# Kernel optimization log

Hardware: AMD Instinct MI355X
Metric: run time of the kernel (lower is better)

## Reference

```python
import jax, jax.numpy as jnp
import numpy as np

N, E = 50000, 800000
IN_CH, H, OUT_CH, ED, L = 64, 128, 128, 1, 4


def setup_inputs() -> dict:
    key = jax.random.key(0)
    ks = jax.random.split(key, 24)
    s = 0.02
    inp = {
        'h': jax.random.normal(ks[0], (N, IN_CH), jnp.float32),
        'coords': jax.random.normal(ks[1], (N, 3), jnp.float32),
        'edge_attr': jax.random.normal(ks[2], (E, ED), jnp.float32),
        'emb_in_W': jax.random.normal(ks[3], (IN_CH, H), jnp.float32) * s,
        'emb_in_b': jnp.zeros((H,), jnp.float32),
        'emb_out_W': jax.random.normal(ks[4], (H, OUT_CH), jnp.float32) * s,
        'emb_out_b': jnp.zeros((OUT_CH,), jnp.float32),
        # per-layer stacked params
        'eW1': jax.random.normal(ks[5], (L, 2 * H + 1 + ED, H), jnp.float32) * s,
        'eb1': jnp.zeros((L, H), jnp.float32),
        'eW2': jax.random.normal(ks[6], (L, H, H), jnp.float32) * s,
        'eb2': jnp.zeros((L, H), jnp.float32),
        'cW1': jax.random.normal(ks[7], (L, H, H), jnp.float32) * s,
        'cb1': jnp.zeros((L, H), jnp.float32),
        'cWc': jax.random.normal(ks[8], (L, H, 1), jnp.float32) * 0.001,  # xavier gain=0.001, no bias
        'nW1': jax.random.normal(ks[9], (L, 2 * H, H), jnp.float32) * s,
        'nb1': jnp.zeros((L, H), jnp.float32),
        'nW2': jax.random.normal(ks[10], (L, H, H), jnp.float32) * s,
        'nb2': jnp.zeros((L, H), jnp.float32),
        'edge_index': jax.random.randint(ks[11], (2, E), 0, N, jnp.int32),
    }
    return inp


def _egnn_forward(h, coords, edge_attr, emb_in_W, emb_in_b, emb_out_W, emb_out_b,
                  eW1, eb1, eW2, eb2, cW1, cb1, cWc, nW1, nb1, nW2, nb2, edge_index):
    silu = jax.nn.silu
    row, col = edge_index[0], edge_index[1]  # PyG: j=source=row, i=target=col
    # count of incoming edges per target node, for coords_agg='mean'
    counts = jax.ops.segment_sum(jnp.ones((E,), jnp.float32), col, num_segments=N)
    counts = jnp.maximum(counts, 1.0)[:, None]
    h = h @ emb_in_W + emb_in_b
    for l in range(L):
        coord_diff = coords[row] - coords[col]                       # [E,3]
        dist = jnp.sum(coord_diff * coord_diff, axis=-1, keepdims=True)  # [E,1]
        # message: edge MLP on cat(x_i, x_j, dist, edge_attr)
        edge_in = jnp.concatenate([h[col], h[row], dist, edge_attr], axis=-1)
        ef = silu(edge_in @ eW1[l] + eb1[l])
        ef = silu(ef @ eW2[l] + eb2[l])                               # [E,H]
        cw = silu(ef @ cW1[l] + cb1[l]) @ cWc[l]                      # [E,1]
        coord_upd = coord_diff * cw                                   # [E,3]
        # aggregate to target nodes
        agg_feat = jax.ops.segment_sum(ef, col, num_segments=N)       # [N,H]
        agg_coord = jax.ops.segment_sum(coord_upd, col, num_segments=N) / counts
        # node update (residual)
        node_in = jnp.concatenate([h, agg_feat], axis=-1)
        upd = silu(node_in @ nW1[l] + nb1[l]) @ nW2[l] + nb2[l]
        h = h + upd
        coords = coords + agg_coord
    h = h @ emb_out_W + emb_out_b
    return h, coords


def reference(h, coords, edge_attr, emb_in_W, emb_in_b, emb_out_W, emb_out_b,
              eW1, eb1, eW2, eb2, cW1, cb1, cWc, nW1, nb1, nW2, nb2, edge_index):
    return _egnn_forward(h, coords, edge_attr, emb_in_W, emb_in_b, emb_out_W, emb_out_b,
                         eW1, eb1, eW2, eb2, cW1, cb1, cWc, nW1, nb1, nW2, nb2, edge_index)
```

## Files before the change

kernel.cpp:

```cpp
#include <hip/hip_runtime.h>

constexpr int Nn = 50000;
constexpr int Ee = 800000;
constexpr int EF_STR  = 136;
constexpr int NIN_STR = 264;
constexpr int HIN_STR = 72;
constexpr int NB_SCAN = (Nn + 255) / 256;

typedef short s8v __attribute__((ext_vector_type(8)));
typedef float f4v __attribute__((ext_vector_type(4)));

__device__ __forceinline__ ushort f2bf(float f) {
    uint u = __float_as_uint(f);
    uint r = (u + 0x7FFFu + ((u >> 16) & 1u)) >> 16;
    return (ushort)r;
}
__device__ __forceinline__ ushort f2bf_t(float f) {
    return (ushort)(__float_as_uint(f) >> 16);
}
__device__ __forceinline__ float bf2f(ushort s) {
    return __uint_as_float(((uint)s) << 16);
}
__device__ __forceinline__ float silu_f(float x) {
    return x * __fdividef(1.0f, 1.0f + __expf(-x));
}
__device__ __forceinline__ uint pack2bf_t(float lo, float hi) {
    return __builtin_amdgcn_perm(__float_as_uint(hi), __float_as_uint(lo), 0x07060302u);
}
__device__ __forceinline__ uint pack2bf_r(float lo, float hi) {
    uint a = __float_as_uint(lo) + 0x8000u;
    uint b = __float_as_uint(hi) + 0x8000u;
    return __builtin_amdgcn_perm(b, a, 0x07060302u);
}

__device__ __forceinline__ void swz_one(const float* src, ushort* dst, int K, int lstride, int KC, int idx)
{
    int per = KC * 4096;
    int l = idx / per, r = idx % per;
    int fb = r >> 9, rem = r & 511;
    int lane = rem >> 3, jj = rem & 7;
    int kc = fb >> 3, t = fb & 7;
    int k = kc * 32 + ((lane >> 4) << 3) + jj;
    int n = t * 16 + (lane & 15);
    float v = (k < K) ? src[(size_t)l * lstride + (size_t)k * 128 + n] : 0.0f;
    dst[idx] = f2bf(v);
}
__global__ void __launch_bounds__(256) k_swz_all(
    const float* __restrict__ eW1, const float* __restrict__ eW2, const float* __restrict__ cW1,
    const float* __restrict__ nW1, const float* __restrict__ nW2,
    const float* __restrict__ inW, const float* __restrict__ outW,
    ushort* __restrict__ oT, ushort* __restrict__ oM,
    ushort* __restrict__ o2, ushort* __restrict__ o3,
    ushort* __restrict__ o4, ushort* __restrict__ o5,
    ushort* __restrict__ o6, ushort* __restrict__ o7)
{
    int gid = blockIdx.x * 256 + threadIdx.x;
    if (gid < 65536)       swz_one(eW1,         oT, 128, 33024, 4, gid);
    else if (gid < 131072) swz_one(eW1 + 16384, oM, 128, 33024, 4, gid - 65536);
    else if (gid < 196608) swz_one(eW2, o2, 128, 16384, 4, gid - 131072);
    else if (gid < 262144) swz_one(cW1, o3, 128, 16384, 4, gid - 196608);
    else if (gid < 393216) swz_one(nW1, o4, 256, 32768, 8, gid - 262144);
    else if (gid < 458752) swz_one(nW2, o5, 128, 16384, 4, gid - 393216);
    else if (gid < 466944) swz_one(inW, o6, 64, 8192, 2, gid - 458752);
    else if (gid < 483328) swz_one(outW, o7, 128, 16384, 4, gid - 466944);
}

__global__ void __launch_bounds__(256) k_count(const int* __restrict__ eidx, int* __restrict__ ecnt)
{
    int e = blockIdx.x * 256 + threadIdx.x;
    atomicAdd(&ecnt[eidx[Ee + e]], 1);
}

__global__ void __launch_bounds__(256) k_bsum(const int* __restrict__ ecnt, int* __restrict__ bsum)
{
    __shared__ int ws[4];
    int tid = threadIdx.x, lane = tid & 63, w = tid >> 6;
    int i = blockIdx.x * 256 + tid;
    int x = (i < Nn) ? ecnt[i] : 0;
    #pragma unroll
    for (int off = 1; off < 64; off <<= 1) x += __shfl_xor(x, off, 64);
    if (lane == 0) ws[w] = x;
    __syncthreads();
    if (tid == 0) bsum[blockIdx.x] = ws[0] + ws[1] + ws[2] + ws[3];
}
__global__ void __launch_bounds__(256) k_bscan(int* __restrict__ bsum)
{
    __shared__ int ws[4];
    int tid = threadIdx.x, lane = tid & 63, w = tid >> 6;
    int x = (tid < NB_SCAN) ? bsum[tid] : 0;
    int s = x;
    #pragma unroll
    for (int off = 1; off < 64; off <<= 1) {
        int t = __shfl_up(s, off, 64);
        if (lane >= off) s += t;
    }
    if (lane == 63) ws[w] = s;
    __syncthreads();
    if (tid == 0) { int a = 0; for (int k = 0; k < 4; k++) { int t = ws[k]; ws[k] = a; a += t; } }
    __syncthreads();
    int excl = ws[w] + s - x;
    if (tid < NB_SCAN) bsum[tid] = excl;
}
__global__ void __launch_bounds__(256) k_cursor(const int* __restrict__ ecnt,
                                               const int* __restrict__ boff, int* __restrict__ cursor)
{
    __shared__ int ws[4];
    int tid = threadIdx.x, lane = tid & 63, w = tid >> 6;
    int i = blockIdx.x * 256 + tid;
    int x = (i < Nn) ? ecnt[i] : 0;
    int s = x;
    #pragma unroll
    for (int off = 1; off < 64; off <<= 1) {
        int t = __shfl_up(s, off, 64);
        if (lane >= off) s += t;
    }
    if (lane == 63) ws[w] = s;
// ... 75 lines not shown
            }
        }
    }
}

__global__ void __launch_bounds__(512, 2) k_uv(
    const ushort* __restrict__ hbf,
    const ushort* __restrict__ topW, const ushort* __restrict__ midW,
    const float* __restrict__ b1, ushort* __restrict__ uvb)
{
    __shared__ alignas(16) ushort s_h[64 * EF_STR];
    const int tid = threadIdx.x;
    const int nb = blockIdx.x * 64;
    #pragma unroll
    for (int i = 0; i < 2; i++) {
        int idx = i * 512 + tid;
        int e = idx >> 4, ch = idx & 15;
        int node = nb + e;
        uint4 v = make_uint4(0, 0, 0, 0);
        if (node < Nn) v = *(const uint4*)(hbf + (size_t)node * 128 + ch * 8);
        *(uint4*)(s_h + e * EF_STR + ch * 8) = v;
    }
    __syncthreads();
    const int lane = tid & 63, wave = tid >> 6;
    const int m = lane & 15, quad = lane >> 4;
    const int ws2 = wave >> 2, wt = wave & 3;
    const int rbase = ws2 * 32;
    f4v au[2][2], av[2][2];
    #pragma unroll
    for (int ct = 0; ct < 2; ct++) {
        float4 bb = *(const float4*)(b1 + (wt * 2 + ct) * 16 + quad * 4);
        au[0][ct] = (f4v){bb.x, bb.y, bb.z, bb.w};
        au[1][ct] = au[0][ct];
        av[0][ct] = (f4v){0,0,0,0};
        av[1][ct] = (f4v){0,0,0,0};
    }
    const ushort* tBase = topW + wt * 1024 + (size_t)lane * 8;
    const ushort* mBase = midW + wt * 1024 + (size_t)lane * 8;
    #pragma unroll
    for (int kc = 0; kc < 4; kc++) {
        s8v t0 = *(const s8v*)(tBase + kc * 4096);
        s8v t1 = *(const s8v*)(tBase + kc * 4096 + 512);
        s8v m0 = *(const s8v*)(mBase + kc * 4096);
        s8v m1 = *(const s8v*)(mBase + kc * 4096 + 512);
        #pragma unroll
        for (int nt = 0; nt < 2; nt++) {
            s8v bf = *(const s8v*)(s_h + (rbase + nt * 16 + m) * EF_STR + kc * 32 + quad * 8);
            au[nt][0] = __builtin_amdgcn_mfma_f32_16x16x32_bf16(t0, bf, au[nt][0], 0, 0, 0);
            au[nt][1] = __builtin_amdgcn_mfma_f32_16x16x32_bf16(t1, bf, au[nt][1], 0, 0, 0);
            av[nt][0] = __builtin_amdgcn_mfma_f32_16x16x32_bf16(m0, bf, av[nt][0], 0, 0, 0);
            av[nt][1] = __builtin_amdgcn_mfma_f32_16x16x32_bf16(m1, bf, av[nt][1], 0, 0, 0);
        }
    }
    #pragma unroll
    for (int nt = 0; nt < 2; nt++) {
        int node = nb + rbase + nt * 16 + m;
        if (node < Nn) {
            #pragma unroll
            for (int ct = 0; ct < 2; ct++) {
                int colb = (wt * 2 + ct) * 16 + quad * 4;
                uint2 pu; pu.x = pack2bf_r(au[nt][ct][0], au[nt][ct][1]);
                          pu.y = pack2bf_r(au[nt][ct][2], au[nt][ct][3]);
                *(uint2*)(uvb + (size_t)node * 256 + colb) = pu;
                uint2 pv; pv.x = pack2bf_r(av[nt][ct][0], av[nt][ct][1]);
                          pv.y = pack2bf_r(av[nt][ct][2], av[nt][ct][3]);
                *(uint2*)(uvb + (size_t)node * 256 + 128 + colb) = pv;
            }
        }
    }
}

__device__ __forceinline__ uint uv_term(uint uw, uint vw, float dist, float attr,
                                        const float* wdp, const float* wap, int j)
{
    float2 w2d = *(const float2*)(wdp + 2 * j);
    float2 w2a = *(const float2*)(wap + 2 * j);
    float lo = __uint_as_float(uw << 16) + __uint_as_float(vw << 16)
             + dist * w2d.x + attr * w2a.x;
    float hi = __uint_as_float(uw & 0xFFFF0000u) + __uint_as_float(vw & 0xFFFF0000u)
             + dist * w2d.y + attr * w2a.y;
    return pack2bf_t(silu_f(lo), silu_f(hi));
}

__global__ void __launch_bounds__(512, 8) k_edge(
    const float* __restrict__ cbuf,
    const int* __restrict__ srow, const int* __restrict__ scol, const float* __restrict__ sattr,
    const ushort* __restrict__ uvb,
    const float* __restrict__ wd, const float* __restrict__ wa,
    const ushort* __restrict__ w2s, const float* __restrict__ b2,
    const ushort* __restrict__ cw1s, const float* __restrict__ cb1,
    const float* __restrict__ cwc,
    float* __restrict__ agg_feat, float* __restrict__ agg_coord)
{
    __shared__ alignas(16) ushort s_a[64 * EF_STR];
    __shared__ alignas(16) ushort s_b[64 * EF_STR];
    __shared__ alignas(16) float  s_t[64 * 20];
    __shared__ int   s_col[64];
    __shared__ float s_cd[64 * 3];

    const int tid = threadIdx.x;
    const int eb = blockIdx.x * 64;

    const int e = tid >> 3, ch = tid & 7;
    const int myrow = srow[eb + e];
    const int mycol = scol[eb + e];
    const float attr = sattr[eb + e];
    const ushort* up = uvb + (size_t)mycol * 256 + ch * 16;
    const ushort* vp = uvb + (size_t)myrow * 256 + 128 + ch * 16;
    uint4 ua = *(const uint4*)up;
    uint4 ub = *(const uint4*)(up + 8);
    uint4 va = *(const uint4*)vp;
    uint4 vb = *(const uint4*)(vp + 8);

    if (tid < 64) {
        int rw = srow[eb + tid], cl = scol[eb + tid];
        s_col[tid] = cl;
        float d0 = cbuf[rw * 3 + 0] - cbuf[cl * 3 + 0];
        float d1 = cbuf[rw * 3 + 1] - cbuf[cl * 3 + 1];
        float d2 = cbuf[rw * 3 + 2] - cbuf[cl * 3 + 2];
        s_cd[tid * 3 + 0] = d0; s_cd[tid * 3 + 1] = d1; s_cd[tid * 3 + 2] = d2;
        s_t[tid * 20 + 16] = d0 * d0 + d1 * d1 + d2 * d2;
    }
    __syncthreads();

    {
        const float dist = s_t[e * 20 + 16];
        const float* wdp = wd + ch * 16;
        const float* wap = wa + ch * 16;
        uint4 q0, q1;
        q0.x = uv_term(ua.x, va.x, dist, attr, wdp, wap, 0);
        q0.y = uv_term(ua.y, va.y, dist, attr, wdp, wap, 1);
        q0.z = uv_term(ua.z, va.z, dist, attr, wdp, wap, 2);
        q0.w = uv_term(ua.w, va.w, dist, attr, wdp, wap, 3);
        *(uint4*)(s_a + e * EF_STR + ch * 16) = q0;
        q1.x = uv_term(ub.x, vb.x, dist, attr, wdp, wap, 4);
        q1.y = uv_term(ub.y, vb.y, dist, attr, wdp, wap, 5);
        q1.z = uv_term(ub.z, vb.z, dist, attr, wdp, wap, 6);
        q1.w = uv_term(ub.w, vb.w, dist, attr, wdp, wap, 7);
        *(uint4*)(s_a + e * EF_STR + ch * 16 + 8) = q1;
    }
    __syncthreads();

    const int lane = tid & 63, wave = tid >> 6;
    const int m = lane & 15, quad = lane >> 4;
    const int ws2 = wave >> 2, wt = wave & 3;
    const int rbase = ws2 * 32;

    {
        f4v acc2[2][2];
        #pragma unroll
        for (int tt = 0; tt < 2; tt++) {
            float4 bb = *(const float4*)(b2 + (wt * 2 + tt) * 16 + quad * 4);
            acc2[0][tt] = (f4v){bb.x, bb.y, bb.z, bb.w};
            acc2[1][tt] = acc2[0][tt];
        }
        const ushort* bBase = w2s + wt * 1024 + (size_t)lane * 8;
        #pragma unroll
        for (int kc = 0; kc < 4; kc++) {
            s8v b0 = *(const s8v*)(bBase + kc * 4096);
            s8v b1v = *(const s8v*)(bBase + kc * 4096 + 512);
            #pragma unroll
            for (int mt = 0; mt < 2; mt++) {
                s8v a = *(const s8v*)(s_a + (rbase + mt * 16 + m) * EF_STR + kc * 32 + quad * 8);
                acc2[mt][0] = __builtin_amdgcn_mfma_f32_16x16x32_bf16(b0, a, acc2[mt][0], 0, 0, 0);
                acc2[mt][1] = __builtin_amdgcn_mfma_f32_16x16x32_bf16(b1v, a, acc2[mt][1], 0, 0, 0);
            }
        }
        #pragma unroll
        for (int mt = 0; mt < 2; mt++)
            #pragma unroll
            for (int tt = 0; tt < 2; tt++) {
                uint2 pk;
                pk.x = pack2bf_t(silu_f(acc2[mt][tt][0]), silu_f(acc2[mt][tt][1]));
                pk.y = pack2bf_t(silu_f(acc2[mt][tt][2]), silu_f(acc2[mt][tt][3]));
                *(uint2*)(s_b + (rbase + mt * 16 + m) * EF_STR + (wt * 2 + tt) * 16 + quad * 4) = pk;
            }
    }
    __syncthreads();

    {
        f4v acc3[2][2];
        #pragma unroll
        for (int tt = 0; tt < 2; tt++) {
            float4 bb = *(const float4*)(cb1 + (wt * 2 + tt) * 16 + quad * 4);
            acc3[0][tt] = (f4v){bb.x, bb.y, bb.z, bb.w};
            acc3[1][tt] = acc3[0][tt];
        }
        const ushort* bBase = cw1s + wt * 1024 + (size_t)lane * 8;
        #pragma unroll
        for (int kc = 0; kc < 4; kc++) {
            s8v b0 = *(const s8v*)(bBase + kc * 4096);
            s8v b1v = *(const s8v*)(bBase + kc * 4096 + 512);
            #pragma unroll
            for (int mt = 0; mt < 2; mt++) {
                s8v a = *(const s8v*)(s_b + (rbase + mt * 16 + m) * EF_STR + kc * 32 + quad * 8);
                acc3[mt][0] = __builtin_amdgcn_mfma_f32_16x16x32_bf16(b0, a, acc3[mt][0], 0, 0, 0);
                acc3[mt][1] = __builtin_amdgcn_mfma_f32_16x16x32_bf16(b1v, a, acc3[mt][1], 0, 0, 0);
            }
        }
        float p0 = 0.0f, p1 = 0.0f;
        #pragma unroll
        for (int tt = 0; tt < 2; tt++) {
            float4 wc = *(const float4*)(cwc + (wt * 2 + tt) * 16 + quad * 4);
            p0 += silu_f(acc3[0][tt][0]) * wc.x + silu_f(acc3[0][tt][1]) * wc.y
                + silu_f(acc3[0][tt][2]) * wc.z + silu_f(acc3[0][tt][3]) * wc.w;
            p1 += silu_f(acc3[1][tt][0]) * wc.x + silu_f(acc3[1][tt][1]) * wc.y
                + silu_f(acc3[1][tt][2]) * wc.z + silu_f(acc3[1][tt][3]) * wc.w;
        }
        p0 += __shfl_xor(p0, 16, 64);
        p0 += __shfl_xor(p0, 32, 64);
        p1 += __shfl_xor(p1, 16, 64);
        p1 += __shfl_xor(p1, 32, 64);
        if (quad == 0) {
            s_t[(rbase + m) * 20 + wt] = p0;
            s_t[(rbase + 16 + m) * 20 + wt] = p1;
        }
    }
    __syncthreads();

    if (tid < 64) {
        float cw = s_t[tid * 20 + 0] + s_t[tid * 20 + 1] + s_t[tid * 20 + 2] + s_t[tid * 20 + 3];
        int cn = s_col[tid];
        unsafeAtomicAdd(&agg_coord[cn * 3 + 0], s_cd[tid * 3 + 0] * cw);
        unsafeAtomicAdd(&agg_coord[cn * 3 + 1], s_cd[tid * 3 + 1] * cw);
        unsafeAtomicAdd(&agg_coord[cn * 3 + 2], s_cd[tid * 3 + 2] * cw);
    }
    {
        int j = tid & 127;
        int e0 = (tid >> 7) * 16;
        float accv = 0.0f; int cur = s_col[e0];
        #pragma unroll 4
        for (int ee = e0; ee < e0 + 16; ee++) {
            int c = s_col[ee];
            if (c != cur) {
                unsafeAtomicAdd(&agg_feat[(size_t)cur * 128 + j], accv);
                accv = 0.0f; cur = c;
            }
            accv += bf2f(s_b[ee * EF_STR + j]);
        }
        unsafeAtomicAdd(&agg_feat[(size_t)cur * 128 + j], accv);
    }
}

__global__ void __launch_bounds__(512, 6) k_node(
    float* __restrict__ hbuf, ushort* __restrict__ hbf, float* __restrict__ cbuf,
    float* __restrict__ agg_feat, float* __restrict__ agg_coord,
    const int* __restrict__ ecnt,
    const ushort* __restrict__ w1s, const float* __restrict__ b1,
    const ushort* __restrict__ w2s, const float* __restrict__ b2)
{
    __shared__ alignas(16) ushort s_nin[64 * NIN_STR];
    __shared__ alignas(16) ushort s_t1[64 * EF_STR];
    const int tid = threadIdx.x;
    const int nb = blockIdx.x * 64;

    #pragma unroll
    for (int i = 0; i < 2; i++) {
        int idx = i * 512 + tid;
        int e = idx >> 4, ch = idx & 15;
        int node = nb + e;
        uint4 v = make_uint4(0, 0, 0, 0);
        if (node < Nn) v = *(const uint4*)(hbf + (size_t)node * 128 + ch * 8);
        *(uint4*)(s_nin + e * NIN_STR + ch * 8) = v;
    }
    #pragma unroll
    for (int i = 0; i < 4; i++) {
        int idx = i * 512 + tid;
        int e = idx >> 5, ch = idx & 31;
        int node = nb + e;
        float4 f = make_float4(0.f, 0.f, 0.f, 0.f);
        if (node < Nn) {
            f = *(const float4*)(agg_feat + (size_t)node * 128 + ch * 4);
            *(float4*)(agg_feat + (size_t)node * 128 + ch * 4) = make_float4(0.f, 0.f, 0.f, 0.f);
        }
        uint2 pk; pk.x = pack2bf_t(f.x, f.y); pk.y = pack2bf_t(f.z, f.w);
        *(uint2*)(s_nin + e * NIN_STR + 128 + ch * 4) = pk;
    }
    if (tid < 64) {
        int n = nb + tid;
        if (n < Nn) {
            float c = (float)ecnt[n]; c = (c < 1.0f) ? 1.0f : c;
            float inv = __fdividef(1.0f, c);
            cbuf[n * 3 + 0] += agg_coord[n * 3 + 0] * inv;
            cbuf[n * 3 + 1] += agg_coord[n * 3 + 1] * inv;
            cbuf[n * 3 + 2] += agg_coord[n * 3 + 2] * inv;
            agg_coord[n * 3 + 0] = 0.f; agg_coord[n * 3 + 1] = 0.f; agg_coord[n * 3 + 2] = 0.f;
        }
    }
    __syncthreads();

    const int lane = tid & 63, wave = tid >> 6;
    const int m = lane & 15, quad = lane >> 4;
    const int ws2 = wave >> 2, wt = wave & 3;
    const int rbase = ws2 * 32;

    {
        f4v acc[2][2];
        #pragma unroll
        for (int ct = 0; ct < 2; ct++) {
            float4 bb = *(const float4*)(b1 + (wt * 2 + ct) * 16 + quad * 4);
            acc[0][ct] = (f4v){bb.x, bb.y, bb.z, bb.w};
            acc[1][ct] = acc[0][ct];
        }
        const ushort* aBase = w1s + wt * 1024 + (size_t)lane * 8;
        #pragma unroll
        for (int kc = 0; kc < 8; kc++) {
            s8v a0 = *(const s8v*)(aBase + kc * 4096);
            s8v a1 = *(const s8v*)(aBase + kc * 4096 + 512);
            #pragma unroll
            for (int nt = 0; nt < 2; nt++) {
                s8v bf = *(const s8v*)(s_nin + (rbase + nt * 16 + m) * NIN_STR + kc * 32 + quad * 8);
                acc[nt][0] = __builtin_amdgcn_mfma_f32_16x16x32_bf16(a0, bf, acc[nt][0], 0, 0, 0);
                acc[nt][1] = __builtin_amdgcn_mfma_f32_16x16x32_bf16(a1, bf, acc[nt][1], 0, 0, 0);
            }
        }
        #pragma unroll
        for (int nt = 0; nt < 2; nt++) {
            int row = rbase + nt * 16 + m;
            #pragma unroll
            for (int ct = 0; ct < 2; ct++) {
                int colb = (wt * 2 + ct) * 16 + quad * 4;
                float v0 = silu_f(acc[nt][ct][0]);
                float v1 = silu_f(acc[nt][ct][1]);
// ... 97 lines not shown
        if (node < Nn) {
            #pragma unroll
            for (int ct = 0; ct < 2; ct++) {
                int colb = (wt * 2 + ct) * 16 + quad * 4;
                float4 o = make_float4(acc[nt][ct][0], acc[nt][ct][1],
                                       acc[nt][ct][2], acc[nt][ct][3]);
                *(float4*)(out + (size_t)node * 128 + colb) = o;
            }
        }
    }
}

extern "C" void kernel_launch(void* const* d_in, const int* in_sizes, int n_in,
                              void* d_out, int out_size, void* d_ws, size_t ws_size,
                              hipStream_t stream)
{
    const float* h_in      = (const float*)d_in[0];
    const float* coords    = (const float*)d_in[1];
    const float* edge_attr = (const float*)d_in[2];
    const float* emb_in_W  = (const float*)d_in[3];
    const float* emb_in_b  = (const float*)d_in[4];
    const float* emb_out_W = (const float*)d_in[5];
    const float* emb_out_b = (const float*)d_in[6];
    const float* eW1 = (const float*)d_in[7];
    const float* eb1 = (const float*)d_in[8];
    const float* eW2 = (const float*)d_in[9];
    const float* eb2 = (const float*)d_in[10];
    const float* cW1 = (const float*)d_in[11];
    const float* cb1 = (const float*)d_in[12];
    const float* cWc = (const float*)d_in[13];
    const float* nW1 = (const float*)d_in[14];
    const float* nb1 = (const float*)d_in[15];
    const float* nW2 = (const float*)d_in[16];
    const float* nb2 = (const float*)d_in[17];
    const int*  eidx = (const int*)d_in[18];

    size_t off = 0;
    char* base = (char*)d_ws;
    auto alloc = [&](size_t bytes) -> char* {
        char* p = base + off;
        off += (bytes + 255) & ~(size_t)255;
        return p;
    };
    float*  hbuf      = (float*)alloc((size_t)Nn * 128 * 4);
    ushort* hbf       = (ushort*)alloc((size_t)Nn * 128 * 2);
    ushort* uvb       = (ushort*)alloc((size_t)Nn * 256 * 2);
    float*  cbuf      = (float*)alloc((size_t)Nn * 3 * 4);
    int*    ecnt      = (int*)alloc((size_t)Nn * 4);
    int*    cursor    = (int*)alloc((size_t)Nn * 4);
    int*    bsum      = (int*)alloc((size_t)NB_SCAN * 4);
    int*    srow      = (int*)alloc((size_t)Ee * 4);
    int*    scol      = (int*)alloc((size_t)Ee * 4);
    float*  sattr     = (float*)alloc((size_t)Ee * 4);
    float*  agg_feat  = (float*)alloc((size_t)Nn * 128 * 4);
    float*  agg_coord = (float*)alloc((size_t)Nn * 3 * 4);
    ushort* eW1tops   = (ushort*)alloc((size_t)4 * 16384 * 2);
    ushort* eW1mids   = (ushort*)alloc((size_t)4 * 16384 * 2);
    ushort* eW2s      = (ushort*)alloc((size_t)4 * 16384 * 2);
    ushort* cW1s      = (ushort*)alloc((size_t)4 * 16384 * 2);
    ushort* nW1s      = (ushort*)alloc((size_t)4 * 32768 * 2);
    ushort* nW2s      = (ushort*)alloc((size_t)4 * 16384 * 2);
    ushort* eInWs     = (ushort*)alloc((size_t)8192 * 2);
    ushort* eOutWs    = (ushort*)alloc((size_t)16384 * 2);

    k_swz_all<<<483328 / 256, 256, 0, stream>>>(
        eW1, eW2, cW1, nW1, nW2, emb_in_W, emb_out_W,
        eW1tops, eW1mids, eW2s, cW1s, nW1s, nW2s, eInWs, eOutWs);

    hipMemsetAsync(ecnt, 0, (size_t)Nn * 4, stream);
    k_count<<<Ee / 256, 256, 0, stream>>>(eidx, ecnt);
    k_bsum<<<NB_SCAN, 256, 0, stream>>>(ecnt, bsum);
    k_bscan<<<1, 256, 0, stream>>>(bsum);
    k_cursor<<<NB_SCAN, 256, 0, stream>>>(ecnt, bsum, cursor);
    k_scatter<<<Ee / 256, 256, 0, stream>>>(eidx, edge_attr, cursor, srow, scol, sattr);
    k_emb<<<(Nn + 63) / 64, 512, 0, stream>>>(h_in, coords, eInWs, emb_in_b, hbuf, hbf, cbuf);

    hipMemsetAsync(agg_feat, 0, (size_t)Nn * 128 * 4, stream);
    hipMemsetAsync(agg_coord, 0, (size_t)Nn * 3 * 4, stream);

    for (int l = 0; l < 4; l++) {
        k_uv<<<(Nn + 63) / 64, 512, 0, stream>>>(
            hbf, eW1tops + (size_t)l * 16384, eW1mids + (size_t)l * 16384,
            eb1 + l * 128, uvb);
        k_edge<<<Ee / 64, 512, 0, stream>>>(
            cbuf, srow, scol, sattr, uvb,
            eW1 + ((size_t)l * 258 + 256) * 128,
            eW1 + ((size_t)l * 258 + 257) * 128,
            eW2s + (size_t)l * 16384, eb2 + l * 128,
            cW1s + (size_t)l * 16384, cb1 + l * 128,
            cWc + l * 128,
            agg_feat, agg_coord);
        k_node<<<(Nn + 63) / 64, 512, 0, stream>>>(
            hbuf, hbf, cbuf, agg_feat, agg_coord, ecnt,
            nW1s + (size_t)l * 32768, nb1 + l * 128,
            nW2s + (size_t)l * 16384, nb2 + l * 128);
    }
    k_emb_out<<<(Nn + 63) / 64, 512, 0, stream>>>(hbf, cbuf, eOutWs, emb_out_b, (float*)d_out);
}
```

Before: 1.642 ms.

## Make edge kernel persistent and prefetch next tile's gathers during compute

The edge kernel becomes a persistent grid-stride loop over 64-edge tiles, launched with a fixed 2048 blocks. Each iteration issues the next tile's index, coordinate and uv gathers into registers, so global latency overlaps the current tile's MFMA work. Per-tile metadata (target column, coordinate diffs) is double-buffered in shared memory, and the barriers become lighter LDS-only waits. The risks are higher register pressure (launch bounds lowered from 8 to 6), lower occupancy, and some tail imbalance, since 12500 tiles do not divide evenly over 2048 blocks.

```diff
diff --git a/kernel.cpp b/kernel.cpp
--- a/kernel.cpp
+++ b/kernel.cpp
@@ -32,6 +32,9 @@
     uint b = __float_as_uint(hi) + 0x8000u;
     return __builtin_amdgcn_perm(b, a, 0x07060302u);
 }
+
+#define LBAR() do { asm volatile("s_waitcnt lgkmcnt(0)" ::: "memory"); \
+                    __builtin_amdgcn_s_barrier(); } while (0)
 
 __device__ __forceinline__ void swz_one(const float* src, ushort* dst, int K, int lstride, int KC, int idx)
 {
@@ -273,7 +276,7 @@
     return pack2bf_t(silu_f(lo), silu_f(hi));
 }
 
-__global__ void __launch_bounds__(512, 8) k_edge(
+__global__ void __launch_bounds__(512, 6) k_edge(
     const float* __restrict__ cbuf,
     const int* __restrict__ srow, const int* __restrict__ scol, const float* __restrict__ sattr,
     const ushort* __restrict__ uvb,
@@ -285,151 +288,170 @@
 {
     __shared__ alignas(16) ushort s_a[64 * EF_STR];
     __shared__ alignas(16) ushort s_b[64 * EF_STR];
-    __shared__ alignas(16) float  s_t[64 * 20];
-    __shared__ int   s_col[64];
-    __shared__ float s_cd[64 * 3];
+    __shared__ alignas(16) float  s_t[64 * 4];
+    __shared__ int   s_col[2][64];
+    __shared__ float s_cd[2][64 * 3];
 
     const int tid = threadIdx.x;
-    const int eb = blockIdx.x * 64;
-
     const int e = tid >> 3, ch = tid & 7;
-    const int myrow = srow[eb + e];
-    const int mycol = scol[eb + e];
-    const float attr = sattr[eb + e];
-    const ushort* up = uvb + (size_t)mycol * 256 + ch * 16;
-    const ushort* vp = uvb + (size_t)myrow * 256 + 128 + ch * 16;
-    uint4 ua = *(const uint4*)up;
-    uint4 ub = *(const uint4*)(up + 8);
-    uint4 va = *(const uint4*)vp;
-    uint4 vb = *(const uint4*)(vp + 8);
-
-    if (tid < 64) {
-        int rw = srow[eb + tid], cl = scol[eb + tid];
-        s_col[tid] = cl;
-        float d0 = cbuf[rw * 3 + 0] - cbuf[cl * 3 + 0];
-        float d1 = cbuf[rw * 3 + 1] - cbuf[cl * 3 + 1];
-        float d2 = cbuf[rw * 3 + 2] - cbuf[cl * 3 + 2];
-        s_cd[tid * 3 + 0] = d0; s_cd[tid * 3 + 1] = d1; s_cd[tid * 3 + 2] = d2;
-        s_t[tid * 20 + 16] = d0 * d0 + d1 * d1 + d2 * d2;
-    }
-    __syncthreads();
-
-    {
-        const float dist = s_t[e * 20 + 16];
-        const float* wdp = wd + ch * 16;
-        const float* wap = wa + ch * 16;
-        uint4 q0, q1;
-        q0.x = uv_term(ua.x, va.x, dist, attr, wdp, wap, 0);
-        q0.y = uv_term(ua.y, va.y, dist, attr, wdp, wap, 1);
-        q0.z = uv_term(ua.z, va.z, dist, attr, wdp, wap, 2);
-        q0.w = uv_term(ua.w, va.w, dist, attr, wdp, wap, 3);
-        *(uint4*)(s_a + e * EF_STR + ch * 16) = q0;
-        q1.x = uv_term(ub.x, vb.x, dist, attr, wdp, wap, 4);
-        q1.y = uv_term(ub.y, vb.y, dist, attr, wdp, wap, 5);
-        q1.z = uv_term(ub.z, vb.z, dist, attr, wdp, wap, 6);
-        q1.w = uv_term(ub.w, vb.w, dist, attr, wdp, wap, 7);
-        *(uint4*)(s_a + e * EF_STR + ch * 16 + 8) = q1;
-    }
-    __syncthreads();
-
     const int lane = tid & 63, wave = tid >> 6;
     const int m = lane & 15, quad = lane >> 4;
     const int ws2 = wave >> 2, wt = wave & 3;
     const int rbase = ws2 * 32;
-
+    constexpr int NT = Ee / 64;
+
+    int t = blockIdx.x;
+    int eb = t * 64;
+    int myrow = srow[eb + e], mycol = scol[eb + e];
+    float attr = sattr[eb + e];
+    float cr0 = cbuf[myrow * 3 + 0], cr1 = cbuf[myrow * 3 + 1], cr2 = cbuf[myrow * 3 + 2];
+    float cc0 = cbuf[mycol * 3 + 0], cc1 = cbuf[mycol * 3 + 1], cc2 = cbuf[mycol * 3 + 2];
+    uint4 ua, ub, va, vb;
     {
-        f4v acc2[2][2];
-        #pragma unroll
-        for (int tt = 0; tt < 2; tt++) {
-            float4 bb = *(const float4*)(b2 + (wt * 2 + tt) * 16 + quad * 4);
-            acc2[0][tt] = (f4v){bb.x, bb.y, bb.z, bb.w};
-            acc2[1][tt] = acc2[0][tt];
-        }
-        const ushort* bBase = w2s + wt * 1024 + (size_t)lane * 8;
-        #pragma unroll
-        for (int kc = 0; kc < 4; kc++) {
-            s8v b0 = *(const s8v*)(bBase + kc * 4096);
-            s8v b1v = *(const s8v*)(bBase + kc * 4096 + 512);
-            #pragma unroll
-            for (int mt = 0; mt < 2; mt++) {
-                s8v a = *(const s8v*)(s_a + (rbase + mt * 16 + m) * EF_STR + kc * 32 + quad * 8);
-                acc2[mt][0] = __builtin_amdgcn_mfma_f32_16x16x32_bf16(b0, a, acc2[mt][0], 0, 0, 0);
-                acc2[mt][1] = __builtin_amdgcn_mfma_f32_16x16x32_bf16(b1v, a, acc2[mt][1], 0, 0, 0);
-            }
-        }
-        #pragma unroll
-        for (int mt = 0; mt < 2; mt++)
+        const ushort* up = uvb + (size_t)mycol * 256 + ch * 16;
+        const ushort* vp = uvb + (size_t)myrow * 256 + 128 + ch * 16;
+        ua = *(const uint4*)up;
+        ub = *(const uint4*)(up + 8);
+        va = *(const uint4*)vp;
+        vb = *(const uint4*)(vp + 8);
+    }
+
+    int buf = 0;
+    for (; t < NT; t += gridDim.x, buf ^= 1) {
+        {
+            float d0 = cr0 - cc0, d1 = cr1 - cc1, d2 = cr2 - cc2;
+            float dist = d0 * d0 + d1 * d1 + d2 * d2;
+            if (ch == 0) {
+                s_col[buf][e] = mycol;
+                s_cd[buf][e * 3 + 0] = d0; s_cd[buf][e * 3 + 1] = d1; s_cd[buf][e * 3 + 2] = d2;
+            }
+            const float* wdp = wd + ch * 16;
+            const float* wap = wa + ch * 16;
+            uint4 q0, q1;
+            q0.x = uv_term(ua.x, va.x, dist, attr, wdp, wap, 0);
+            q0.y = uv_term(ua.y, va.y, dist, attr, wdp, wap, 1);
+            q0.z = uv_term(ua.z, va.z, dist, attr, wdp, wap, 2);
+            q0.w = uv_term(ua.w, va.w, dist, attr, wdp, wap, 3);
+            *(uint4*)(s_a + e * EF_STR + ch * 16) = q0;
+            q1.x = uv_term(ub.x, vb.x, dist, attr, wdp, wap, 4);
+            q1.y = uv_term(ub.y, vb.y, dist, attr, wdp, wap, 5);
+            q1.z = uv_term(ub.z, vb.z, dist, attr, wdp, wap, 6);
+            q1.w = uv_term(ub.w, vb.w, dist, attr, wdp, wap, 7);
+            *(uint4*)(s_a + e * EF_STR + ch * 16 + 8) = q1;
+        }
+        {
+            int nxt = t + gridDim.x;
+            int nt2 = (nxt < NT) ? nxt : t;
+            int neb = nt2 * 64;
+            int nrow = srow[neb + e], ncol = scol[neb + e];
+            float nattr = sattr[neb + e];
+            cr0 = cbuf[nrow * 3 + 0]; cr1 = cbuf[nrow * 3 + 1]; cr2 = cbuf[nrow * 3 + 2];
+            cc0 = cbuf[ncol * 3 + 0]; cc1 = cbuf[ncol * 3 + 1]; cc2 = cbuf[ncol * 3 + 2];
+            const ushort* up = uvb + (size_t)ncol * 256 + ch * 16;
+            const ushort* vp = uvb + (size_t)nrow * 256 + 128 + ch * 16;
+            ua = *(const uint4*)up;
+            ub = *(const uint4*)(up + 8);
+            va = *(const uint4*)vp;
+            vb = *(const uint4*)(vp + 8);
+            myrow = nrow; mycol = ncol; attr = nattr;
+        }
+        LBAR();
+
+        {
+            f4v acc2[2][2];
             #pragma unroll
             for (int tt = 0; tt < 2; tt++) {
-                uint2 pk;
-                pk.x = pack2bf_t(silu_f(acc2[mt][tt][0]), silu_f(acc2[mt][tt][1]));
-                pk.y = pack2bf_t(silu_f(acc2[mt][tt][2]), silu_f(acc2[mt][tt][3]));
-                *(uint2*)(s_b + (rbase + mt * 16 + m) * EF_STR + (wt * 2 + tt) * 16 + quad * 4) = pk;
-            }
-    }
-    __syncthreads();
-
-    {
-        f4v acc3[2][2];
-        #pragma unroll
-        for (int tt = 0; tt < 2; tt++) {
-            float4 bb = *(const float4*)(cb1 + (wt * 2 + tt) * 16 + quad * 4);
-            acc3[0][tt] = (f4v){bb.x, bb.y, bb.z, bb.w};
-            acc3[1][tt] = acc3[0][tt];
-        }
-        const ushort* bBase = cw1s + wt * 1024 + (size_t)lane * 8;
-        #pragma unroll
-        for (int kc = 0; kc < 4; kc++) {
-            s8v b0 = *(const s8v*)(bBase + kc * 4096);
-            s8v b1v = *(const s8v*)(bBase + kc * 4096 + 512);
-            #pragma unroll
-            for (int mt = 0; mt < 2; mt++) {
-                s8v a = *(const s8v*)(s_b + (rbase + mt * 16 + m) * EF_STR + kc * 32 + quad * 8);
-                acc3[mt][0] = __builtin_amdgcn_mfma_f32_16x16x32_bf16(b0, a, acc3[mt][0], 0, 0, 0);
-                acc3[mt][1] = __builtin_amdgcn_mfma_f32_16x16x32_bf16(b1v, a, acc3[mt][1], 0, 0, 0);
-            }
-        }
-        float p0 = 0.0f, p1 = 0.0f;
-        #pragma unroll
-        for (int tt = 0; tt < 2; tt++) {
-            float4 wc = *(const float4*)(cwc + (wt * 2 + tt) * 16 + quad * 4);
-            p0 += silu_f(acc3[0][tt][0]) * wc.x + silu_f(acc3[0][tt][1]) * wc.y
-                + silu_f(acc3[0][tt][2]) * wc.z + silu_f(acc3[0][tt][3]) * wc.w;
-            p1 += silu_f(acc3[1][tt][0]) * wc.x + silu_f(acc3[1][tt][1]) * wc.y
-                + silu_f(acc3[1][tt][2]) * wc.z + silu_f(acc3[1][tt][3]) * wc.w;
-        }
-        p0 += __shfl_xor(p0, 16, 64);
-        p0 += __shfl_xor(p0, 32, 64);
-        p1 += __shfl_xor(p1, 16, 64);
-        p1 += __shfl_xor(p1, 32, 64);
-        if (quad == 0) {
-            s_t[(rbase + m) * 20 + wt] = p0;
-            s_t[(rbase + 16 + m) * 20 + wt] = p1;
-        }
-    }
-    __syncthreads();
-
-    if (tid < 64) {
-        float cw = s_t[tid * 20 + 0] + s_t[tid * 20 + 1] + s_t[tid * 20 + 2] + s_t[tid * 20 + 3];
-        int cn = s_col[tid];
-        unsafeAtomicAdd(&agg_coord[cn * 3 + 0], s_cd[tid * 3 + 0] * cw);
-        unsafeAtomicAdd(&agg_coord[cn * 3 + 1], s_cd[tid * 3 + 1] * cw);
-        unsafeAtomicAdd(&agg_coord[cn * 3 + 2], s_cd[tid * 3 + 2] * cw);
-    }
-    {
-        int j = tid & 127;
-        int e0 = (tid >> 7) * 16;
-        float accv = 0.0f; int cur = s_col[e0];
-        #pragma unroll 4
-        for (int ee = e0; ee < e0 + 16; ee++) {
-            int c = s_col[ee];
-            if (c != cur) {
-                unsafeAtomicAdd(&agg_feat[(size_t)cur * 128 + j], accv);
-                accv = 0.0f; cur = c;
-            }
-            accv += bf2f(s_b[ee * EF_STR + j]);
-        }
-        unsafeAtomicAdd(&agg_feat[(size_t)cur * 128 + j], accv);
+                float4 bb = *(const float4*)(b2 + (wt * 2 + tt) * 16 + quad * 4);
+                acc2[0][tt] = (f4v){bb.x, bb.y, bb.z, bb.w};
+                acc2[1][tt] = acc2[0][tt];
+            }
+            const ushort* bBase = w2s + wt * 1024 + (size_t)lane * 8;
+            #pragma unroll
+            for (int kc = 0; kc < 4; kc++) {
+                s8v b0 = *(const s8v*)(bBase + kc * 4096);
+                s8v b1v = *(const s8v*)(bBase + kc * 4096 + 512);
+                #pragma unroll
+                for (int mt = 0; mt < 2; mt++) {
+                    s8v a = *(const s8v*)(s_a + (rbase + mt * 16 + m) * EF_STR + kc * 32 + quad * 8);
+                    acc2[mt][0] = __builtin_amdgcn_mfma_f32_16x16x32_bf16(b0, a, acc2[mt][0], 0, 0, 0);
+                    acc2[mt][1] = __builtin_amdgcn_mfma_f32_16x16x32_bf16(b1v, a, acc2[mt][1], 0, 0, 0);
+                }
+            }
+            #pragma unroll
+            for (int mt = 0; mt < 2; mt++)
+                #pragma unroll
+                for (int tt = 0; tt < 2; tt++) {
+                    uint2 pk;
+                    pk.x = pack2bf_t(silu_f(acc2[mt][tt][0]), silu_f(acc2[mt][tt][1]));
+                    pk.y = pack2bf_t(silu_f(acc2[mt][tt][2]), silu_f(acc2[mt][tt][3]));
+                    *(uint2*)(s_b + (rbase + mt * 16 + m) * EF_STR + (wt * 2 + tt) * 16 + quad * 4) = pk;
+                }
+        }
+        LBAR();
+
+        {
+            f4v acc3[2][2];
+            #pragma unroll
+            for (int tt = 0; tt < 2; tt++) {
+                float4 bb = *(const float4*)(cb1 + (wt * 2 + tt) * 16 + quad * 4);
+                acc3[0][tt] = (f4v){bb.x, bb.y, bb.z, bb.w};
+                acc3[1][tt] = acc3[0][tt];
+            }
+            const ushort* bBase = cw1s + wt * 1024 + (size_t)lane * 8;
+            #pragma unroll
+            for (int kc = 0; kc < 4; kc++) {
+                s8v b0 = *(const s8v*)(bBase + kc * 4096);
+                s8v b1v = *(const s8v*)(bBase + kc * 4096 + 512);
+                #pragma unroll
+                for (int mt = 0; mt < 2; mt++) {
+                    s8v a = *(const s8v*)(s_b + (rbase + mt * 16 + m) * EF_STR + kc * 32 + quad * 8);
+                    acc3[mt][0] = __builtin_amdgcn_mfma_f32_16x16x32_bf16(b0, a, acc3[mt][0], 0, 0, 0);
+                    acc3[mt][1] = __builtin_amdgcn_mfma_f32_16x16x32_bf16(b1v, a, acc3[mt][1], 0, 0, 0);
+                }
+            }
+            float p0 = 0.0f, p1 = 0.0f;
+            #pragma unroll
+            for (int tt = 0; tt < 2; tt++) {
+                float4 wc = *(const float4*)(cwc + (wt * 2 + tt) * 16 + quad * 4);
+                p0 += silu_f(acc3[0][tt][0]) * wc.x + silu_f(acc3[0][tt][1]) * wc.y
+                    + silu_f(acc3[0][tt][2]) * wc.z + silu_f(acc3[0][tt][3]) * wc.w;
+                p1 += silu_f(acc3[1][tt][0]) * wc.x + silu_f(acc3[1][tt][1]) * wc.y
+                    + silu_f(acc3[1][tt][2]) * wc.z + silu_f(acc3[1][tt][3]) * wc.w;
+            }
+            p0 += __shfl_xor(p0, 16, 64);
+            p0 += __shfl_xor(p0, 32, 64);
+            p1 += __shfl_xor(p1, 16, 64);
+            p1 += __shfl_xor(p1, 32, 64);
+            if (quad == 0) {
+                s_t[(rbase + m) * 4 + wt] = p0;
+                s_t[(rbase + 16 + m) * 4 + wt] = p1;
+            }
+        }
+        LBAR();
+
+        if (tid < 64) {
+            float4 pt = *(const float4*)(s_t + tid * 4);
+            float cw = pt.x + pt.y + pt.z + pt.w;
+            int cn = s_col[buf][tid];
+            unsafeAtomicAdd(&agg_coord[cn * 3 + 0], s_cd[buf][tid * 3 + 0] * cw);
+            unsafeAtomicAdd(&agg_coord[cn * 3 + 1], s_cd[buf][tid * 3 + 1] * cw);
+            unsafeAtomicAdd(&agg_coord[cn * 3 + 2], s_cd[buf][tid * 3 + 2] * cw);
+        }
+        {
+            int j = tid & 127;
+            int e0 = (tid >> 7) * 16;
+            float accv = 0.0f; int cur = s_col[buf][e0];
+            #pragma unroll 4
+            for (int ee = e0; ee < e0 + 16; ee++) {
+                int c = s_col[buf][ee];
+                if (c != cur) {
+                    unsafeAtomicAdd(&agg_feat[(size_t)cur * 128 + j], accv);
+                    accv = 0.0f; cur = c;
+                }
+                accv += bf2f(s_b[ee * EF_STR + j]);
+            }
+            unsafeAtomicAdd(&agg_feat[(size_t)cur * 128 + j], accv);
+        }
     }
 }
 
@@ -693,7 +715,7 @@
         k_uv<<<(Nn + 63) / 64, 512, 0, stream>>>(
             hbf, eW1tops + (size_t)l * 16384, eW1mids + (size_t)l * 16384,
             eb1 + l * 128, uvb);
-        k_edge<<<Ee / 64, 512, 0, stream>>>(
+        k_edge<<<2048, 512, 0, stream>>>(
             cbuf, srow, scol, sattr, uvb,
             eW1 + ((size_t)l * 258 + 256) * 128,
             eW1 + ((size_t)l * 258 + 257) * 128,
```

New measurement: 2.626 ms. +60.0%, slower.

## Process 128 edges per block in edge kernel, reuse single LDS buffer

Applied to the files above, without the earlier changes.

Each edge-kernel block now handles 128 edges instead of 64, so every wave runs 4 MFMA row tiles against each loaded weight fragment. This doubles reuse of the weight loads from global memory and halves the block count. The second LDS buffer is dropped: the layer-2 outputs overwrite the input buffer after an extra barrier, which keeps shared memory usage about the same. The costs are more accumulator registers per thread (which may reduce occupancy under the launch bounds of 8) and one more synchronisation.

```diff
diff --git a/kernel.cpp b/kernel.cpp
--- a/kernel.cpp
+++ b/kernel.cpp
@@ -283,67 +283,69 @@
     const float* __restrict__ cwc,
     float* __restrict__ agg_feat, float* __restrict__ agg_coord)
 {
-    __shared__ alignas(16) ushort s_a[64 * EF_STR];
-    __shared__ alignas(16) ushort s_b[64 * EF_STR];
-    __shared__ alignas(16) float  s_t[64 * 20];
-    __shared__ int   s_col[64];
-    __shared__ float s_cd[64 * 3];
+    __shared__ alignas(16) ushort s_a[128 * EF_STR];
+    __shared__ alignas(16) float  s_p[128 * 4];
+    __shared__ float s_dist[128];
+    __shared__ int   s_col[128];
+    __shared__ float s_cd[128 * 3];
 
     const int tid = threadIdx.x;
-    const int eb = blockIdx.x * 64;
-
-    const int e = tid >> 3, ch = tid & 7;
-    const int myrow = srow[eb + e];
-    const int mycol = scol[eb + e];
-    const float attr = sattr[eb + e];
-    const ushort* up = uvb + (size_t)mycol * 256 + ch * 16;
-    const ushort* vp = uvb + (size_t)myrow * 256 + 128 + ch * 16;
-    uint4 ua = *(const uint4*)up;
-    uint4 ub = *(const uint4*)(up + 8);
-    uint4 va = *(const uint4*)vp;
-    uint4 vb = *(const uint4*)(vp + 8);
-
-    if (tid < 64) {
+    const int eb = blockIdx.x * 128;
+
+    if (tid < 128) {
         int rw = srow[eb + tid], cl = scol[eb + tid];
         s_col[tid] = cl;
         float d0 = cbuf[rw * 3 + 0] - cbuf[cl * 3 + 0];
         float d1 = cbuf[rw * 3 + 1] - cbuf[cl * 3 + 1];
         float d2 = cbuf[rw * 3 + 2] - cbuf[cl * 3 + 2];
         s_cd[tid * 3 + 0] = d0; s_cd[tid * 3 + 1] = d1; s_cd[tid * 3 + 2] = d2;
-        s_t[tid * 20 + 16] = d0 * d0 + d1 * d1 + d2 * d2;
+        s_dist[tid] = d0 * d0 + d1 * d1 + d2 * d2;
     }
     __syncthreads();
 
     {
-        const float dist = s_t[e * 20 + 16];
-        const float* wdp = wd + ch * 16;
-        const float* wap = wa + ch * 16;
-        uint4 q0, q1;
-        q0.x = uv_term(ua.x, va.x, dist, attr, wdp, wap, 0);
-        q0.y = uv_term(ua.y, va.y, dist, attr, wdp, wap, 1);
-        q0.z = uv_term(ua.z, va.z, dist, attr, wdp, wap, 2);
-        q0.w = uv_term(ua.w, va.w, dist, attr, wdp, wap, 3);
-        *(uint4*)(s_a + e * EF_STR + ch * 16) = q0;
-        q1.x = uv_term(ub.x, vb.x, dist, attr, wdp, wap, 4);
-        q1.y = uv_term(ub.y, vb.y, dist, attr, wdp, wap, 5);
-        q1.z = uv_term(ub.z, vb.z, dist, attr, wdp, wap, 6);
-        q1.w = uv_term(ub.w, vb.w, dist, attr, wdp, wap, 7);
-        *(uint4*)(s_a + e * EF_STR + ch * 16 + 8) = q1;
+        const int e = tid >> 2, ch = tid & 3;
+        int row = srow[eb + e], col = scol[eb + e];
+        float attr = sattr[eb + e];
+        float dist = s_dist[e];
+        const ushort* up = uvb + (size_t)col * 256 + ch * 32;
+        const ushort* vp = uvb + (size_t)row * 256 + 128 + ch * 32;
+        #pragma unroll
+        for (int hf = 0; hf < 2; hf++) {
+            uint4 ua = *(const uint4*)(up + hf * 16);
+            uint4 ub = *(const uint4*)(up + hf * 16 + 8);
+            uint4 va = *(const uint4*)(vp + hf * 16);
+            uint4 vb = *(const uint4*)(vp + hf * 16 + 8);
+            const float* wdp = wd + ch * 32 + hf * 16;
+            const float* wap = wa + ch * 32 + hf * 16;
+            uint4 q0, q1;
+            q0.x = uv_term(ua.x, va.x, dist, attr, wdp, wap, 0);
+            q0.y = uv_term(ua.y, va.y, dist, attr, wdp, wap, 1);
+            q0.z = uv_term(ua.z, va.z, dist, attr, wdp, wap, 2);
+            q0.w = uv_term(ua.w, va.w, dist, attr, wdp, wap, 3);
+            *(uint4*)(s_a + e * EF_STR + ch * 32 + hf * 16) = q0;
+            q1.x = uv_term(ub.x, vb.x, dist, attr, wdp, wap, 4);
+            q1.y = uv_term(ub.y, vb.y, dist, attr, wdp, wap, 5);
+            q1.z = uv_term(ub.z, vb.z, dist, attr, wdp, wap, 6);
+            q1.w = uv_term(ub.w, vb.w, dist, attr, wdp, wap, 7);
+            *(uint4*)(s_a + e * EF_STR + ch * 32 + hf * 16 + 8) = q1;
+        }
     }
     __syncthreads();
 
     const int lane = tid & 63, wave = tid >> 6;
     const int m = lane & 15, quad = lane >> 4;
     const int ws2 = wave >> 2, wt = wave & 3;
-    const int rbase = ws2 * 32;
-
+    const int rbase = ws2 * 64;
+
+    f4v acc2[4][2];
     {
-        f4v acc2[2][2];
         #pragma unroll
         for (int tt = 0; tt < 2; tt++) {
             float4 bb = *(const float4*)(b2 + (wt * 2 + tt) * 16 + quad * 4);
-            acc2[0][tt] = (f4v){bb.x, bb.y, bb.z, bb.w};
-            acc2[1][tt] = acc2[0][tt];
+            f4v b4 = (f4v){bb.x, bb.y, bb.z, bb.w};
+            #pragma unroll
+            for (int mt = 0; mt < 4; mt++) acc2[mt][tt] = b4;
         }
         const ushort* bBase = w2s + wt * 1024 + (size_t)lane * 8;
         #pragma unroll
@@ -351,31 +353,33 @@
             s8v b0 = *(const s8v*)(bBase + kc * 4096);
             s8v b1v = *(const s8v*)(bBase + kc * 4096 + 512);
             #pragma unroll
-            for (int mt = 0; mt < 2; mt++) {
+            for (int mt = 0; mt < 4; mt++) {
                 s8v a = *(const s8v*)(s_a + (rbase + mt * 16 + m) * EF_STR + kc * 32 + quad * 8);
                 acc2[mt][0] = __builtin_amdgcn_mfma_f32_16x16x32_bf16(b0, a, acc2[mt][0], 0, 0, 0);
                 acc2[mt][1] = __builtin_amdgcn_mfma_f32_16x16x32_bf16(b1v, a, acc2[mt][1], 0, 0, 0);
             }
         }
-        #pragma unroll
-        for (int mt = 0; mt < 2; mt++)
-            #pragma unroll
-            for (int tt = 0; tt < 2; tt++) {
-                uint2 pk;
-                pk.x = pack2bf_t(silu_f(acc2[mt][tt][0]), silu_f(acc2[mt][tt][1]));
-                pk.y = pack2bf_t(silu_f(acc2[mt][tt][2]), silu_f(acc2[mt][tt][3]));
-                *(uint2*)(s_b + (rbase + mt * 16 + m) * EF_STR + (wt * 2 + tt) * 16 + quad * 4) = pk;
-            }
-    }
+    }
+    __syncthreads();
+    #pragma unroll
+    for (int mt = 0; mt < 4; mt++)
+        #pragma unroll
+        for (int tt = 0; tt < 2; tt++) {
+            uint2 pk;
+            pk.x = pack2bf_t(silu_f(acc2[mt][tt][0]), silu_f(acc2[mt][tt][1]));
+            pk.y = pack2bf_t(silu_f(acc2[mt][tt][2]), silu_f(acc2[mt][tt][3]));
+            *(uint2*)(s_a + (rbase + mt * 16 + m) * EF_STR + (wt * 2 + tt) * 16 + quad * 4) = pk;
+        }
     __syncthreads();
 
     {
-        f4v acc3[2][2];
+        f4v acc3[4][2];
         #pragma unroll
         for (int tt = 0; tt < 2; tt++) {
             float4 bb = *(const float4*)(cb1 + (wt * 2 + tt) * 16 + quad * 4);
-            acc3[0][tt] = (f4v){bb.x, bb.y, bb.z, bb.w};
-            acc3[1][tt] = acc3[0][tt];
+            f4v b4 = (f4v){bb.x, bb.y, bb.z, bb.w};
+            #pragma unroll
+            for (int mt = 0; mt < 4; mt++) acc3[mt][tt] = b4;
         }
         const ushort* bBase = cw1s + wt * 1024 + (size_t)lane * 8;
         #pragma unroll
@@ -383,34 +387,30 @@
             s8v b0 = *(const s8v*)(bBase + kc * 4096);
             s8v b1v = *(const s8v*)(bBase + kc * 4096 + 512);
             #pragma unroll
-            for (int mt = 0; mt < 2; mt++) {
-                s8v a = *(const s8v*)(s_b + (rbase + mt * 16 + m) * EF_STR + kc * 32 + quad * 8);
+            for (int mt = 0; mt < 4; mt++) {
+                s8v a = *(const s8v*)(s_a + (rbase + mt * 16 + m) * EF_STR + kc * 32 + quad * 8);
                 acc3[mt][0] = __builtin_amdgcn_mfma_f32_16x16x32_bf16(b0, a, acc3[mt][0], 0, 0, 0);
                 acc3[mt][1] = __builtin_amdgcn_mfma_f32_16x16x32_bf16(b1v, a, acc3[mt][1], 0, 0, 0);
             }
         }
-        float p0 = 0.0f, p1 = 0.0f;
-        #pragma unroll
-        for (int tt = 0; tt < 2; tt++) {
-            float4 wc = *(const float4*)(cwc + (wt * 2 + tt) * 16 + quad * 4);
-            p0 += silu_f(acc3[0][tt][0]) * wc.x + silu_f(acc3[0][tt][1]) * wc.y
-                + silu_f(acc3[0][tt][2]) * wc.z + silu_f(acc3[0][tt][3]) * wc.w;
-            p1 += silu_f(acc3[1][tt][0]) * wc.x + silu_f(acc3[1][tt][1]) * wc.y
-                + silu_f(acc3[1][tt][2]) * wc.z + silu_f(acc3[1][tt][3]) * wc.w;
-        }
-        p0 += __shfl_xor(p0, 16, 64);
-        p0 += __shfl_xor(p0, 32, 64);
-        p1 += __shfl_xor(p1, 16, 64);
-        p1 += __shfl_xor(p1, 32, 64);
-        if (quad == 0) {
-            s_t[(rbase + m) * 20 + wt] = p0;
-            s_t[(rbase + 16 + m) * 20 + wt] = p1;
-        }
-    }
-    __syncthreads();
-
-    if (tid < 64) {
-        float cw = s_t[tid * 20 + 0] + s_t[tid * 20 + 1] + s_t[tid * 20 + 2] + s_t[tid * 20 + 3];
+        float4 wc0 = *(const float4*)(cwc + (wt * 2 + 0) * 16 + quad * 4);
+        float4 wc1 = *(const float4*)(cwc + (wt * 2 + 1) * 16 + quad * 4);
+        #pragma unroll
+        for (int mt = 0; mt < 4; mt++) {
+            float p = silu_f(acc3[mt][0][0]) * wc0.x + silu_f(acc3[mt][0][1]) * wc0.y
+                    + silu_f(acc3[mt][0][2]) * wc0.z + silu_f(acc3[mt][0][3]) * wc0.w
+                    + silu_f(acc3[mt][1][0]) * wc1.x + silu_f(acc3[mt][1][1]) * wc1.y
+                    + silu_f(acc3[mt][1][2]) * wc1.z + silu_f(acc3[mt][1][3]) * wc1.w;
+            p += __shfl_xor(p, 16, 64);
+            p += __shfl_xor(p, 32, 64);
+            if (quad == 0) s_p[(rbase + mt * 16 + m) * 4 + wt] = p;
+        }
+    }
+    __syncthreads();
+
+    if (tid < 128) {
+        float4 pt = *(const float4*)(s_p + tid * 4);
+        float cw = pt.x + pt.y + pt.z + pt.w;
         int cn = s_col[tid];
         unsafeAtomicAdd(&agg_coord[cn * 3 + 0], s_cd[tid * 3 + 0] * cw);
         unsafeAtomicAdd(&agg_coord[cn * 3 + 1], s_cd[tid * 3 + 1] * cw);
@@ -418,16 +418,16 @@
     }
     {
         int j = tid & 127;
-        int e0 = (tid >> 7) * 16;
+        int e0 = (tid >> 7) * 32;
         float accv = 0.0f; int cur = s_col[e0];
         #pragma unroll 4
-        for (int ee = e0; ee < e0 + 16; ee++) {
+        for (int ee = e0; ee < e0 + 32; ee++) {
             int c = s_col[ee];
             if (c != cur) {
                 unsafeAtomicAdd(&agg_feat[(size_t)cur * 128 + j], accv);
                 accv = 0.0f; cur = c;
             }
-            accv += bf2f(s_b[ee * EF_STR + j]);
+            accv += bf2f(s_a[ee * EF_STR + j]);
         }
         unsafeAtomicAdd(&agg_feat[(size_t)cur * 128 + j], accv);
     }
@@ -693,7 +693,7 @@
         k_uv<<<(Nn + 63) / 64, 512, 0, stream>>>(
             hbf, eW1tops + (size_t)l * 16384, eW1mids + (size_t)l * 16384,
             eb1 + l * 128, uvb);
-        k_edge<<<Ee / 64, 512, 0, stream>>>(
+        k_edge<<<Ee / 128, 512, 0, stream>>>(
             cbuf, srow, scol, sattr, uvb,
             eW1 + ((size_t)l * 258 + 256) * 128,
             eW1 + ((size_t)l * 258 + 257) * 128,
```

Result: faster. 1.579 ms (-3.8%).
